# Kernel tuning notes

Hardware: AMD Instinct MI355X
Metric: run time of the kernel (lower is better)

## Reference

```python
import jax, jax.numpy as jnp
import numpy as np

N = 262144
MUL0, MUL1, MUL2 = 128, 64, 32          # multiplicities of 0e, 1o, 2e
D0, D1, D2 = MUL0, MUL1 * 3, MUL2 * 5   # flat dims: 128, 192, 160
NG = MUL1 + MUL2                        # 96 gate scalars (0e)
NS = MUL0 + NG                          # 224 scalar outputs of the Linear


def _norm2mom_cst(f):
    # e3nn normalize2mom: rescale activation so E_{x~N(0,1)}[f(x)^2] = 1
    xs = np.random.default_rng(0).standard_normal(1_000_000).astype(np.float32)
    return float(1.0 / np.sqrt(np.mean(np.asarray(f(jnp.asarray(xs))) ** 2)))

CST_SILU = _norm2mom_cst(jax.nn.silu)
CST_RELU = _norm2mom_cst(jax.nn.relu)


def setup_inputs() -> dict:
    key = jax.random.key(0)
    k = jax.random.split(key, 5)
    return {
        "x": jax.random.normal(k[0], (N, D0 + D1 + D2), jnp.float32),
        "W0": jax.random.normal(k[1], (MUL0, NS), jnp.float32),
        "b0": jax.random.normal(k[2], (NS,), jnp.float32),
        "W1": jax.random.normal(k[3], (MUL1, MUL1), jnp.float32),
        "W2": jax.random.normal(k[4], (MUL2, MUL2), jnp.float32),
    }


def reference(x, W0, b0, W1, W2):
    n = x.shape[0]
    # split input into irrep blocks: [n,128] 0e, [n,64,3] 1o, [n,32,5] 2e
    x0 = x[:, :D0]
    x1 = x[:, D0:D0 + D1].reshape(n, MUL1, 3)
    x2 = x[:, D0 + D1:].reshape(n, MUL2, 5)
    # e3nn o3.Linear: per-irrep block matmul with 1/sqrt(fan_in) path norm;
    # bias only on scalar (0e) outputs
    s = x0 @ W0 * (1.0 / np.sqrt(MUL0)) + b0                      # [n,224]
    v = jnp.einsum('nim,ij->njm', x1, W1) * (1.0 / np.sqrt(MUL1))  # [n,64,3]
    t = jnp.einsum('nim,ij->njm', x2, W2) * (1.0 / np.sqrt(MUL2))  # [n,32,5]
    # e3nn Gate: silu on the 128 true scalars, relu on the 96 gates,
    # gated irreps multiplied channelwise by their gate scalar
    scalars = CST_SILU * jax.nn.silu(s[:, :MUL0])                  # [n,128]
    gates = CST_RELU * jax.nn.relu(s[:, MUL0:])                    # [n,96]
    gv = (v * gates[:, :MUL1, None]).reshape(n, D1)                # [n,192]
    gt = (t * gates[:, MUL1:, None]).reshape(n, D2)                # [n,160]
    return jnp.concatenate([scalars, gv, gt], axis=-1)            # [n,480]
```

## Files before the change

kernel.cpp:

```cpp
#include <hip/hip_runtime.h>
#include <hip/hip_bf16.h>

#define NROWS   262144
#define DIN     480
#define DOUT    480

#define M_TILE  32
#define XSTR    488

#define CST_SILU 1.6765290f
#define CST_RELU 1.4142135623730951f
#define INV_S128 0.08838834764831845f
#define INV_S64  0.125f
#define INV_S32  0.17677669529663687f

#define WS_FRAGS 66
#define WS_BYTES (WS_FRAGS * 64 * 16)

typedef short bf16x8 __attribute__((ext_vector_type(8)));
typedef float f32x4  __attribute__((ext_vector_type(4)));

__device__ __forceinline__ ushort f2bf(float f) {
    unsigned u = __float_as_uint(f);
    u = (u + 0x7FFFu + ((u >> 16) & 1u)) >> 16;
    return (ushort)u;
}

__device__ __forceinline__ unsigned pk2(float a, float b) {
    __hip_bfloat162 h = __float22bfloat162_rn(float2{a, b});
    return *reinterpret_cast<unsigned*>(&h);
}

__device__ __forceinline__ bf16x8 load_b_frag(const float* __restrict__ W, int ldw,
                                              int kbase, int nbase, int lane) {
    int n  = nbase + (lane & 15);
    int k0 = kbase + ((lane >> 4) << 3);
    bf16x8 f;
#pragma unroll
    for (int e = 0; e < 8; ++e) f[e] = (short)f2bf(W[(k0 + e) * ldw + n]);
    return f;
}

__global__ __launch_bounds__(64) void prep_frags(
        const float* __restrict__ W0, const float* __restrict__ W1,
        const float* __restrict__ W2, ushort* __restrict__ ws) {
    const int b = blockIdx.x, lane = threadIdx.x;
    const int lr = lane & 15, kg = lane >> 4;
    const float* W; int ldw, n, k0;
    if (b < 56)      { W = W0; ldw = 224; n = (b >> 2) * 16 + lr; k0 = (b & 3) * 32 + (kg << 3); }
    else if (b < 64) { int t = b - 56; W = W1; ldw = 64; n = (t >> 1) * 16 + lr; k0 = (t & 1) * 32 + (kg << 3); }
    else             { W = W2; ldw = 32; n = (b - 64) * 16 + lr; k0 = (kg << 3); }
    bf16x8 f;
#pragma unroll
    for (int e = 0; e < 8; ++e) f[e] = (short)f2bf(W[(k0 + e) * ldw + n]);
    *reinterpret_cast<bf16x8*>(ws + (b * 64 + lane) * 8) = f;
}

template <bool PRE>
__global__ __launch_bounds__(256, 4) void percep_kernel(
        const float* __restrict__ x,  const float* __restrict__ W0,
        const float* __restrict__ bias0, const float* __restrict__ W1,
        const float* __restrict__ W2, float* __restrict__ out,
        const ushort* __restrict__ ws) {
    __shared__ __align__(16) ushort xs[M_TILE * XSTR];

    const int tid  = threadIdx.x;
    const int lane = tid & 63;
    const int wid  = tid >> 6;
    const int lr   = lane & 15;
    const int kg   = lane >> 4;
    const int rf   = wid >> 1;
    const int half = wid & 1;
    const int row0 = blockIdx.x * M_TILE;
    const bf16x8* F = reinterpret_cast<const bf16x8*>(ws);

#pragma unroll
    for (int it = 0; it < 4; ++it) {
        int idx = tid + it * 256;
        int row = idx >> 5, c4 = idx & 31;
        const float4 v = reinterpret_cast<const float4*>(x + (row0 + row) * DIN)[c4];
        uint2 o = { pk2(v.x, v.y), pk2(v.z, v.w) };
        *reinterpret_cast<uint2*>(&xs[row * XSTR + c4 * 4]) = o;
    }
#pragma unroll
    for (int it = 0; it < 2; ++it) {
        int idx = tid + it * 256;
        int row = idx >> 4, g = idx & 15;
        const float4* p = reinterpret_cast<const float4*>(x + (row0 + row) * DIN + 128 + 12 * g);
        float4 q0 = p[0], q1 = p[1], q2 = p[2];
        float v[12] = { q0.x, q0.y, q0.z, q0.w, q1.x, q1.y, q1.z, q1.w, q2.x, q2.y, q2.z, q2.w };
#pragma unroll
        for (int m = 0; m < 3; ++m) {
            uint2 o = { pk2(v[m], v[m + 3]), pk2(v[m + 6], v[m + 9]) };
            *reinterpret_cast<uint2*>(&xs[row * XSTR + 128 + 64 * m + 4 * g]) = o;
        }
    }
    {
        int row = tid >> 3, g = tid & 7;
        const float4* p = reinterpret_cast<const float4*>(x + (row0 + row) * DIN + 320 + 20 * g);
        float4 q0 = p[0], q1 = p[1], q2 = p[2], q3 = p[3], q4 = p[4];
        float v[20] = { q0.x, q0.y, q0.z, q0.w, q1.x, q1.y, q1.z, q1.w, q2.x, q2.y, q2.z, q2.w,
                        q3.x, q3.y, q3.z, q3.w, q4.x, q4.y, q4.z, q4.w };
#pragma unroll
        for (int m = 0; m < 5; ++m) {
            uint2 o = { pk2(v[m], v[m + 5]), pk2(v[m + 10], v[m + 15]) };
            *reinterpret_cast<uint2*>(&xs[row * XSTR + 320 + 32 * m + 4 * g]) = o;
        }
    }
    __syncthreads();

    bf16x8 aS[4];
#pragma unroll
    for (int kk = 0; kk < 4; ++kk)
        aS[kk] = *reinterpret_cast<const bf16x8*>(
            &xs[(rf * 16 + lr) * XSTR + kk * 32 + (kg << 3)]);

    f32x4 gV0, gV1, gT;
    const int gt0 = half ? 10 : 8, gt1 = half ? 11 : 9, gt2 = half ? 13 : 12;

    auto s_acc = [&](int st) -> f32x4 {
        f32x4 acc = { 0.f, 0.f, 0.f, 0.f };
#pragma unroll
        for (int kk = 0; kk < 4; ++kk) {
            bf16x8 b = PRE ? F[(st * 4 + kk) * 64 + lane]
                           : load_b_frag(W0, 224, kk * 32, st * 16, lane);
            acc = __builtin_amdgcn_mfma_f32_16x16x32_bf16(aS[kk], b, acc, 0, 0, 0);
        }
        return acc;
    };
    auto gate_tile = [&](int st) -> f32x4 {
        f32x4 acc = s_acc(st);
        float bias = bias0[st * 16 + lr];
        f32x4 g;
#pragma unroll
        for (int r = 0; r < 4; ++r) {
            float s = acc[r] * INV_S128 + bias;
            g[r] = fmaxf(s, 0.f) * CST_RELU;
        }
        return g;
    };
    gV0 = gate_tile(gt0);
    gV1 = gate_tile(gt1);
    gT  = gate_tile(gt2);
#pragma unroll
    for (int t = 0; t < 4; ++t) {
        int st = half * 4 + t;
        f32x4 acc = s_acc(st);
        float bias = bias0[st * 16 + lr];
#pragma unroll
        for (int r = 0; r < 4; ++r) {
            float s = acc[r] * INV_S128 + bias;
            float val = CST_SILU * s * __builtin_amdgcn_rcpf(1.f + __expf(-s));
            out[(row0 + rf * 16 + (kg << 2) + r) * DOUT + st * 16 + lr] = val;
        }
    }

    {
        bf16x8 aV[3][2];
#pragma unroll
        for (int m = 0; m < 3; ++m)
#pragma unroll
            for (int kk = 0; kk < 2; ++kk)
                aV[m][kk] = *reinterpret_cast<const bf16x8*>(
                    &xs[(rf * 16 + lr) * XSTR + 128 + m * 64 + kk * 32 + (kg << 3)]);
#pragma unroll
        for (int jt = 0; jt < 2; ++jt) {
            const int jtg = half * 2 + jt;
            f32x4 a0 = {0,0,0,0}, a1 = {0,0,0,0}, a2 = {0,0,0,0};
#pragma unroll
            for (int kk = 0; kk < 2; ++kk) {
                bf16x8 b = PRE ? F[(56 + jtg * 2 + kk) * 64 + lane]
                               : load_b_frag(W1, 64, kk * 32, jtg * 16, lane);
                a0 = __builtin_amdgcn_mfma_f32_16x16x32_bf16(aV[0][kk], b, a0, 0, 0, 0);
                a1 = __builtin_amdgcn_mfma_f32_16x16x32_bf16(aV[1][kk], b, a1, 0, 0, 0);
                a2 = __builtin_amdgcn_mfma_f32_16x16x32_bf16(aV[2][kk], b, a2, 0, 0, 0);
            }
            const f32x4& gv = jt ? gV1 : gV0;
            int j = jtg * 16 + lr;
#pragma unroll
            for (int r = 0; r < 4; ++r) {
                int row = rf * 16 + (kg << 2) + r;
                float g = gv[r] * INV_S64;
                float* po = out + (row0 + row) * DOUT + 128 + 3 * j;
                po[0] = a0[r] * g; po[1] = a1[r] * g; po[2] = a2[r] * g;
            }
        }
    }

    {
        bf16x8 bt = PRE ? F[(64 + half) * 64 + lane]
                        : load_b_frag(W2, 32, 0, half * 16, lane);
        const ushort* base = &xs[(rf * 16 + lr) * XSTR + 320 + (kg << 3)];
        f32x4 z = {0,0,0,0};
        f32x4 a0 = __builtin_amdgcn_mfma_f32_16x16x32_bf16(*reinterpret_cast<const bf16x8*>(base +   0), bt, z, 0, 0, 0);
        f32x4 a1 = __builtin_amdgcn_mfma_f32_16x16x32_bf16(*reinterpret_cast<const bf16x8*>(base +  32), bt, z, 0, 0, 0);
        f32x4 a2 = __builtin_amdgcn_mfma_f32_16x16x32_bf16(*reinterpret_cast<const bf16x8*>(base +  64), bt, z, 0, 0, 0);
        f32x4 a3 = __builtin_amdgcn_mfma_f32_16x16x32_bf16(*reinterpret_cast<const bf16x8*>(base +  96), bt, z, 0, 0, 0);
        f32x4 a4 = __builtin_amdgcn_mfma_f32_16x16x32_bf16(*reinterpret_cast<const bf16x8*>(base + 128), bt, z, 0, 0, 0);
        int j = half * 16 + lr;
#pragma unroll
        for (int r = 0; r < 4; ++r) {
            int row = rf * 16 + (kg << 2) + r;
            float g = gT[r] * INV_S32;
            float* po = out + (row0 + row) * DOUT + 320 + 5 * j;
            po[0] = a0[r] * g; po[1] = a1[r] * g; po[2] = a2[r] * g;
            po[3] = a3[r] * g; po[4] = a4[r] * g;
        }
    }
}

extern "C" void kernel_launch(void* const* d_in, const int* in_sizes, int n_in,
                              void* d_out, int out_size, void* d_ws, size_t ws_size,
                              hipStream_t stream) {
    const float* x  = (const float*)d_in[0];
    const float* W0 = (const float*)d_in[1];
    const float* b0 = (const float*)d_in[2];
    const float* W1 = (const float*)d_in[3];
    const float* W2 = (const float*)d_in[4];
    float* out = (float*)d_out;
    dim3 grid(NROWS / M_TILE), block(256);
    if (ws_size >= WS_BYTES) {
        hipLaunchKernelGGL(prep_frags, dim3(WS_FRAGS), dim3(64), 0, stream, W0, W1, W2, (ushort*)d_ws);
        hipLaunchKernelGGL((percep_kernel<true>), grid, block, 0, stream,
                           x, W0, b0, W1, W2, out, (const ushort*)d_ws);
    } else {
        hipLaunchKernelGGL((percep_kernel<false>), grid, block, 0, stream,
                           x, W0, b0, W1, W2, out, (const ushort*)d_ws);
    }
}
```

Measured before the change: 222.2 us.

## Process four row tiles per block with register prefetch of next tile

Each block now loops over four 32-row tiles, issuing global loads for the next tile into registers before computing the current tile, so input fetch overlaps MFMA and epilogue work. Output stores for the gated vector and tensor parts are grouped into 3- and 5-float struct stores. Occupancy hint drops from 4 to 3 blocks per CU to make room for the 15 float4 prefetch registers, and the grid shrinks fourfold, which may reduce latency hiding from block-level parallelism.

```diff
diff --git a/kernel.cpp b/kernel.cpp
--- a/kernel.cpp
+++ b/kernel.cpp
@@ -6,6 +6,8 @@
 #define DOUT    480
 
 #define M_TILE  32
+#define T_PER_BLOCK 4
+#define GRID    (NROWS / (M_TILE * T_PER_BLOCK))
 #define XSTR    488
 
 #define CST_SILU 1.6765290f
@@ -20,12 +22,14 @@
 typedef short bf16x8 __attribute__((ext_vector_type(8)));
 typedef float f32x4  __attribute__((ext_vector_type(4)));
 
+struct __align__(4) F3 { float a, b, c; };
+struct __align__(4) F5 { float a, b, c, d, e; };
+
 __device__ __forceinline__ ushort f2bf(float f) {
     unsigned u = __float_as_uint(f);
     u = (u + 0x7FFFu + ((u >> 16) & 1u)) >> 16;
     return (ushort)u;
 }
-
 __device__ __forceinline__ unsigned pk2(float a, float b) {
     __hip_bfloat162 h = __float22bfloat162_rn(float2{a, b});
     return *reinterpret_cast<unsigned*>(&h);
@@ -57,7 +61,7 @@
 }
 
 template <bool PRE>
-__global__ __launch_bounds__(256, 4) void percep_kernel(
+__global__ __launch_bounds__(256, 3) void percep_kernel(
         const float* __restrict__ x,  const float* __restrict__ W0,
         const float* __restrict__ bias0, const float* __restrict__ W1,
         const float* __restrict__ W2, float* __restrict__ out,
@@ -71,141 +75,177 @@
     const int kg   = lane >> 4;
     const int rf   = wid >> 1;
     const int half = wid & 1;
-    const int row0 = blockIdx.x * M_TILE;
+    const int base0 = blockIdx.x * (M_TILE * T_PER_BLOCK);
     const bf16x8* F = reinterpret_cast<const bf16x8*>(ws);
 
-#pragma unroll
-    for (int it = 0; it < 4; ++it) {
-        int idx = tid + it * 256;
-        int row = idx >> 5, c4 = idx & 31;
-        const float4 v = reinterpret_cast<const float4*>(x + (row0 + row) * DIN)[c4];
-        uint2 o = { pk2(v.x, v.y), pk2(v.z, v.w) };
-        *reinterpret_cast<uint2*>(&xs[row * XSTR + c4 * 4]) = o;
-    }
-#pragma unroll
-    for (int it = 0; it < 2; ++it) {
-        int idx = tid + it * 256;
-        int row = idx >> 4, g = idx & 15;
-        const float4* p = reinterpret_cast<const float4*>(x + (row0 + row) * DIN + 128 + 12 * g);
-        float4 q0 = p[0], q1 = p[1], q2 = p[2];
-        float v[12] = { q0.x, q0.y, q0.z, q0.w, q1.x, q1.y, q1.z, q1.w, q2.x, q2.y, q2.z, q2.w };
-#pragma unroll
-        for (int m = 0; m < 3; ++m) {
-            uint2 o = { pk2(v[m], v[m + 3]), pk2(v[m + 6], v[m + 9]) };
-            *reinterpret_cast<uint2*>(&xs[row * XSTR + 128 + 64 * m + 4 * g]) = o;
-        }
-    }
-    {
-        int row = tid >> 3, g = tid & 7;
-        const float4* p = reinterpret_cast<const float4*>(x + (row0 + row) * DIN + 320 + 20 * g);
-        float4 q0 = p[0], q1 = p[1], q2 = p[2], q3 = p[3], q4 = p[4];
-        float v[20] = { q0.x, q0.y, q0.z, q0.w, q1.x, q1.y, q1.z, q1.w, q2.x, q2.y, q2.z, q2.w,
-                        q3.x, q3.y, q3.z, q3.w, q4.x, q4.y, q4.z, q4.w };
-#pragma unroll
-        for (int m = 0; m < 5; ++m) {
-            uint2 o = { pk2(v[m], v[m + 5]), pk2(v[m + 10], v[m + 15]) };
-            *reinterpret_cast<uint2*>(&xs[row * XSTR + 320 + 32 * m + 4 * g]) = o;
-        }
-    }
-    __syncthreads();
-
-    bf16x8 aS[4];
-#pragma unroll
-    for (int kk = 0; kk < 4; ++kk)
-        aS[kk] = *reinterpret_cast<const bf16x8*>(
-            &xs[(rf * 16 + lr) * XSTR + kk * 32 + (kg << 3)]);
-
-    f32x4 gV0, gV1, gT;
-    const int gt0 = half ? 10 : 8, gt1 = half ? 11 : 9, gt2 = half ? 13 : 12;
-
-    auto s_acc = [&](int st) -> f32x4 {
-        f32x4 acc = { 0.f, 0.f, 0.f, 0.f };
-#pragma unroll
-        for (int kk = 0; kk < 4; ++kk) {
-            bf16x8 b = PRE ? F[(st * 4 + kk) * 64 + lane]
-                           : load_b_frag(W0, 224, kk * 32, st * 16, lane);
-            acc = __builtin_amdgcn_mfma_f32_16x16x32_bf16(aS[kk], b, acc, 0, 0, 0);
-        }
-        return acc;
+    float4 pr[15];
+
+    auto issue_loads = [&](int row0) {
+#pragma unroll
+        for (int it = 0; it < 4; ++it) {
+            int idx = tid + it * 256;
+            int row = idx >> 5, c4 = idx & 31;
+            pr[it] = reinterpret_cast<const float4*>(x + (row0 + row) * DIN)[c4];
+        }
+#pragma unroll
+        for (int it = 0; it < 2; ++it) {
+            int idx = tid + it * 256;
+            int row = idx >> 4, g = idx & 15;
+            const float4* p = reinterpret_cast<const float4*>(x + (row0 + row) * DIN + 128 + 12 * g);
+            pr[4 + it * 3] = p[0]; pr[5 + it * 3] = p[1]; pr[6 + it * 3] = p[2];
+        }
+        {
+            int row = tid >> 3, g = tid & 7;
+            const float4* p = reinterpret_cast<const float4*>(x + (row0 + row) * DIN + 320 + 20 * g);
+            pr[10] = p[0]; pr[11] = p[1]; pr[12] = p[2]; pr[13] = p[3]; pr[14] = p[4];
+        }
     };
-    auto gate_tile = [&](int st) -> f32x4 {
-        f32x4 acc = s_acc(st);
-        float bias = bias0[st * 16 + lr];
-        f32x4 g;
-#pragma unroll
-        for (int r = 0; r < 4; ++r) {
-            float s = acc[r] * INV_S128 + bias;
-            g[r] = fmaxf(s, 0.f) * CST_RELU;
-        }
-        return g;
+
+    auto convert_to_lds = [&]() {
+#pragma unroll
+        for (int it = 0; it < 4; ++it) {
+            int idx = tid + it * 256;
+            int row = idx >> 5, c4 = idx & 31;
+            uint2 o = { pk2(pr[it].x, pr[it].y), pk2(pr[it].z, pr[it].w) };
+            *reinterpret_cast<uint2*>(&xs[row * XSTR + c4 * 4]) = o;
+        }
+#pragma unroll
+        for (int it = 0; it < 2; ++it) {
+            int idx = tid + it * 256;
+            int row = idx >> 4, g = idx & 15;
+            float v[12] = { pr[4+it*3].x, pr[4+it*3].y, pr[4+it*3].z, pr[4+it*3].w,
+                            pr[5+it*3].x, pr[5+it*3].y, pr[5+it*3].z, pr[5+it*3].w,
+                            pr[6+it*3].x, pr[6+it*3].y, pr[6+it*3].z, pr[6+it*3].w };
+#pragma unroll
+            for (int m = 0; m < 3; ++m) {
+                uint2 o = { pk2(v[m], v[m + 3]), pk2(v[m + 6], v[m + 9]) };
+                *reinterpret_cast<uint2*>(&xs[row * XSTR + 128 + 64 * m + 4 * g]) = o;
+            }
+        }
+        {
+            int row = tid >> 3, g = tid & 7;
+            float v[20] = { pr[10].x, pr[10].y, pr[10].z, pr[10].w,
+                            pr[11].x, pr[11].y, pr[11].z, pr[11].w,
+                            pr[12].x, pr[12].y, pr[12].z, pr[12].w,
+                            pr[13].x, pr[13].y, pr[13].z, pr[13].w,
+                            pr[14].x, pr[14].y, pr[14].z, pr[14].w };
+#pragma unroll
+            for (int m = 0; m < 5; ++m) {
+                uint2 o = { pk2(v[m], v[m + 5]), pk2(v[m + 10], v[m + 15]) };
+                *reinterpret_cast<uint2*>(&xs[row * XSTR + 320 + 32 * m + 4 * g]) = o;
+            }
+        }
     };
-    gV0 = gate_tile(gt0);
-    gV1 = gate_tile(gt1);
-    gT  = gate_tile(gt2);
-#pragma unroll
-    for (int t = 0; t < 4; ++t) {
-        int st = half * 4 + t;
-        f32x4 acc = s_acc(st);
-        float bias = bias0[st * 16 + lr];
-#pragma unroll
-        for (int r = 0; r < 4; ++r) {
-            float s = acc[r] * INV_S128 + bias;
-            float val = CST_SILU * s * __builtin_amdgcn_rcpf(1.f + __expf(-s));
-            out[(row0 + rf * 16 + (kg << 2) + r) * DOUT + st * 16 + lr] = val;
-        }
-    }
-
-    {
-        bf16x8 aV[3][2];
-#pragma unroll
-        for (int m = 0; m < 3; ++m)
-#pragma unroll
-            for (int kk = 0; kk < 2; ++kk)
-                aV[m][kk] = *reinterpret_cast<const bf16x8*>(
-                    &xs[(rf * 16 + lr) * XSTR + 128 + m * 64 + kk * 32 + (kg << 3)]);
-#pragma unroll
-        for (int jt = 0; jt < 2; ++jt) {
-            const int jtg = half * 2 + jt;
-            f32x4 a0 = {0,0,0,0}, a1 = {0,0,0,0}, a2 = {0,0,0,0};
-#pragma unroll
-            for (int kk = 0; kk < 2; ++kk) {
-                bf16x8 b = PRE ? F[(56 + jtg * 2 + kk) * 64 + lane]
-                               : load_b_frag(W1, 64, kk * 32, jtg * 16, lane);
-                a0 = __builtin_amdgcn_mfma_f32_16x16x32_bf16(aV[0][kk], b, a0, 0, 0, 0);
-                a1 = __builtin_amdgcn_mfma_f32_16x16x32_bf16(aV[1][kk], b, a1, 0, 0, 0);
-                a2 = __builtin_amdgcn_mfma_f32_16x16x32_bf16(aV[2][kk], b, a2, 0, 0, 0);
-            }
-            const f32x4& gv = jt ? gV1 : gV0;
-            int j = jtg * 16 + lr;
+
+    auto compute_tile = [&](int row0) {
+        bf16x8 aS[4];
+#pragma unroll
+        for (int kk = 0; kk < 4; ++kk)
+            aS[kk] = *reinterpret_cast<const bf16x8*>(
+                &xs[(rf * 16 + lr) * XSTR + kk * 32 + (kg << 3)]);
+
+        const int orow = row0 + rf * 16 + (kg << 2);
+
+        auto s_acc = [&](int st) -> f32x4 {
+            f32x4 acc = { 0.f, 0.f, 0.f, 0.f };
+#pragma unroll
+            for (int kk = 0; kk < 4; ++kk) {
+                bf16x8 b = PRE ? F[(st * 4 + kk) * 64 + lane]
+                               : load_b_frag(W0, 224, kk * 32, st * 16, lane);
+                acc = __builtin_amdgcn_mfma_f32_16x16x32_bf16(aS[kk], b, acc, 0, 0, 0);
+            }
+            return acc;
+        };
+        auto gate_tile = [&](int st) -> f32x4 {
+            f32x4 acc = s_acc(st);
+            float bias = bias0[st * 16 + lr];
+            f32x4 g;
 #pragma unroll
             for (int r = 0; r < 4; ++r) {
-                int row = rf * 16 + (kg << 2) + r;
-                float g = gv[r] * INV_S64;
-                float* po = out + (row0 + row) * DOUT + 128 + 3 * j;
-                po[0] = a0[r] * g; po[1] = a1[r] * g; po[2] = a2[r] * g;
-            }
-        }
-    }
-
-    {
-        bf16x8 bt = PRE ? F[(64 + half) * 64 + lane]
-                        : load_b_frag(W2, 32, 0, half * 16, lane);
-        const ushort* base = &xs[(rf * 16 + lr) * XSTR + 320 + (kg << 3)];
-        f32x4 z = {0,0,0,0};
-        f32x4 a0 = __builtin_amdgcn_mfma_f32_16x16x32_bf16(*reinterpret_cast<const bf16x8*>(base +   0), bt, z, 0, 0, 0);
-        f32x4 a1 = __builtin_amdgcn_mfma_f32_16x16x32_bf16(*reinterpret_cast<const bf16x8*>(base +  32), bt, z, 0, 0, 0);
-        f32x4 a2 = __builtin_amdgcn_mfma_f32_16x16x32_bf16(*reinterpret_cast<const bf16x8*>(base +  64), bt, z, 0, 0, 0);
-        f32x4 a3 = __builtin_amdgcn_mfma_f32_16x16x32_bf16(*reinterpret_cast<const bf16x8*>(base +  96), bt, z, 0, 0, 0);
-        f32x4 a4 = __builtin_amdgcn_mfma_f32_16x16x32_bf16(*reinterpret_cast<const bf16x8*>(base + 128), bt, z, 0, 0, 0);
-        int j = half * 16 + lr;
-#pragma unroll
-        for (int r = 0; r < 4; ++r) {
-            int row = rf * 16 + (kg << 2) + r;
-            float g = gT[r] * INV_S32;
-            float* po = out + (row0 + row) * DOUT + 320 + 5 * j;
-            po[0] = a0[r] * g; po[1] = a1[r] * g; po[2] = a2[r] * g;
-            po[3] = a3[r] * g; po[4] = a4[r] * g;
-        }
+                float s = acc[r] * INV_S128 + bias;
+                g[r] = fmaxf(s, 0.f) * CST_RELU;
+            }
+            return g;
+        };
+        auto silu_tile = [&](int st) {
+            f32x4 acc = s_acc(st);
+            float bias = bias0[st * 16 + lr];
+#pragma unroll
+            for (int r = 0; r < 4; ++r) {
+                float s = acc[r] * INV_S128 + bias;
+                float val = CST_SILU * s * __builtin_amdgcn_rcpf(1.f + __expf(-s));
+                out[(orow + r) * DOUT + st * 16 + lr] = val;
+            }
+        };
+
+        f32x4 gV0 = gate_tile(half ? 10 : 8);
+        f32x4 gV1 = gate_tile(half ? 11 : 9);
+        f32x4 gT  = gate_tile(half ? 13 : 12);
+        silu_tile(half * 4 + 0);
+        silu_tile(half * 4 + 1);
+        silu_tile(half * 4 + 2);
+        silu_tile(half * 4 + 3);
+
+        {
+            bf16x8 aV[3][2];
+#pragma unroll
+            for (int m = 0; m < 3; ++m)
+#pragma unroll
+                for (int kk = 0; kk < 2; ++kk)
+                    aV[m][kk] = *reinterpret_cast<const bf16x8*>(
+                        &xs[(rf * 16 + lr) * XSTR + 128 + m * 64 + kk * 32 + (kg << 3)]);
+#pragma unroll
+            for (int jt = 0; jt < 2; ++jt) {
+                const int jtg = half * 2 + jt;
+                f32x4 a0 = {0,0,0,0}, a1 = {0,0,0,0}, a2 = {0,0,0,0};
+#pragma unroll
+                for (int kk = 0; kk < 2; ++kk) {
+                    bf16x8 b = PRE ? F[(56 + jtg * 2 + kk) * 64 + lane]
+                                   : load_b_frag(W1, 64, kk * 32, jtg * 16, lane);
+                    a0 = __builtin_amdgcn_mfma_f32_16x16x32_bf16(aV[0][kk], b, a0, 0, 0, 0);
+                    a1 = __builtin_amdgcn_mfma_f32_16x16x32_bf16(aV[1][kk], b, a1, 0, 0, 0);
+                    a2 = __builtin_amdgcn_mfma_f32_16x16x32_bf16(aV[2][kk], b, a2, 0, 0, 0);
+                }
+                const f32x4& gv = jt ? gV1 : gV0;
+                int j = jtg * 16 + lr;
+#pragma unroll
+                for (int r = 0; r < 4; ++r) {
+                    float gg = gv[r] * INV_S64;
+                    F3 o = { a0[r] * gg, a1[r] * gg, a2[r] * gg };
+                    *reinterpret_cast<F3*>(out + (orow + r) * DOUT + 128 + 3 * j) = o;
+                }
+            }
+        }
+
+        {
+            bf16x8 bt = PRE ? F[(64 + half) * 64 + lane]
+                            : load_b_frag(W2, 32, 0, half * 16, lane);
+            const ushort* base = &xs[(rf * 16 + lr) * XSTR + 320 + (kg << 3)];
+            f32x4 z = {0,0,0,0};
+            f32x4 a0 = __builtin_amdgcn_mfma_f32_16x16x32_bf16(*reinterpret_cast<const bf16x8*>(base +   0), bt, z, 0, 0, 0);
+            f32x4 a1 = __builtin_amdgcn_mfma_f32_16x16x32_bf16(*reinterpret_cast<const bf16x8*>(base +  32), bt, z, 0, 0, 0);
+            f32x4 a2 = __builtin_amdgcn_mfma_f32_16x16x32_bf16(*reinterpret_cast<const bf16x8*>(base +  64), bt, z, 0, 0, 0);
+            f32x4 a3 = __builtin_amdgcn_mfma_f32_16x16x32_bf16(*reinterpret_cast<const bf16x8*>(base +  96), bt, z, 0, 0, 0);
+            f32x4 a4 = __builtin_amdgcn_mfma_f32_16x16x32_bf16(*reinterpret_cast<const bf16x8*>(base + 128), bt, z, 0, 0, 0);
+            int j = half * 16 + lr;
+#pragma unroll
+            for (int r = 0; r < 4; ++r) {
+                float gg = gT[r] * INV_S32;
+                F5 o = { a0[r] * gg, a1[r] * gg, a2[r] * gg, a3[r] * gg, a4[r] * gg };
+                *reinterpret_cast<F5*>(out + (orow + r) * DOUT + 320 + 5 * j) = o;
+            }
+        }
+    };
+
+    issue_loads(base0);
+#pragma unroll 1
+    for (int t = 0; t < T_PER_BLOCK; ++t) {
+        convert_to_lds();
+        __syncthreads();
+        if (t + 1 < T_PER_BLOCK)
+            issue_loads(base0 + (t + 1) * M_TILE);
+        compute_tile(base0 + t * M_TILE);
+        __syncthreads();
     }
 }
 
@@ -218,7 +258,7 @@
     const float* W1 = (const float*)d_in[3];
     const float* W2 = (const float*)d_in[4];
     float* out = (float*)d_out;
-    dim3 grid(NROWS / M_TILE), block(256);
+    dim3 grid(GRID), block(256);
     if (ws_size >= WS_BYTES) {
         hipLaunchKernelGGL(prep_frags, dim3(WS_FRAGS), dim3(64), 0, stream, W0, W1, W2, (ushort*)d_ws);
         hipLaunchKernelGGL((percep_kernel<true>), grid, block, 0, stream,
```

Measured after the change: 417.0 us. 87.7% more time.
